# Kernel tuning notes

Measured on AMD Instinct MI355X. Metric: run time of the kernel, lower is better.

The kernel has to match this reference:

```python
import jax, jax.numpy as jnp
import numpy as np

EPS = 1e-8

def _conv(x, w, b=None):
    # NCHW conv, stride 1, SAME padding (k=3, pad=1)
    y = jax.lax.conv_general_dilated(x, w, (1, 1), 'SAME',
                                     dimension_numbers=('NCHW', 'OIHW', 'NCHW'))
    if b is not None:
        y = y + b[None, :, None, None]
    return y

def setup_inputs() -> dict:
    key = jax.random.key(0)
    ks = jax.random.split(key, 6)
    B, C, H, W = 512, 1024, 8, 8
    return {
        'x': jax.random.normal(ks[0], (B, C, H, W), jnp.float32),
        'w1_1': jax.random.normal(ks[1], (1, 1, 3, 3), jnp.float32) * 0.1,
        'w5': jax.random.normal(ks[2], (4, 2, 3, 3), jnp.float32) * 0.1,
        'b5': jax.random.normal(ks[3], (4,), jnp.float32) * 0.1,
        'w6': jax.random.normal(ks[4], (1, 4, 3, 3), jnp.float32) * 0.1,
        'b6': jax.random.normal(ks[5], (1,), jnp.float32) * 0.1,
    }

def reference(x, w1_1, w5, b5, w6, b6):
    B, C, H, W = x.shape  # H == W == 8 by module construction
    m = jnp.max(x, axis=1, keepdims=True)  # [B,1,H,W] channel max
    # 2x2 non-overlapping windows, torch unfold layout -> [B,1,(H/2)*(W/2),4]
    win = m.reshape(B, 1, H // 2, 2, W // 2, 2)
    win = win.transpose(0, 1, 2, 4, 3, 5).reshape(B, 1, (H // 2) * (W // 2), 4)
    # probabilistic pooling: clean inf/nan/negatives, sample per window
    winc = jnp.where(jnp.isinf(win) | jnp.isnan(win) | (win < 0), EPS, win)
    skey = jax.random.key(1)
    idx = jax.random.categorical(skey, winc, axis=-1)  # softmax(winc) multinomial
    mo2 = jnp.take_along_axis(winc, idx[..., None], axis=-1)[..., 0]
    mo2 = mo2.reshape(B, 1, H // 2, W // 2)
    # adaptive max/avg pool (4,4) on 8x8 == 2x2 pooling, reuse windows
    mo3 = win.max(axis=-1).reshape(B, 1, H // 2, W // 2)
    ao4 = win.mean(axis=-1).reshape(B, 1, H // 2, W // 2)
    out2 = 0.1 * mo2 + 0.6 * mo3 + 0.3 * ao4
    out2 = _conv(out2, w1_1)  # bias-free 1->1 conv
    out2 = jax.image.resize(out2, (B, 1, H, W), method='bilinear')  # align_corners=False
    out1 = jnp.concatenate([m, out2], axis=1)  # [B,2,H,W]
    gate = jax.nn.sigmoid(_conv(jax.nn.relu(_conv(out1, w5, b5)), w6, b6))  # [B,1,H,W]
    return jax.nn.relu(x * gate)
```

## Files before the change

kernel.cpp:

```cpp
#include <hip/hip_runtime.h>
#include <math.h>

#define C_DIM 1024
#define HW 64
#define F4_PER_BATCH 16384
#define EPSV 1e-8f
#define TINYF 1.17549435e-38f

typedef float vfloat4 __attribute__((ext_vector_type(4)));

__device__ __forceinline__ void threefry2x32_01(unsigned x0, unsigned x1,
                                                unsigned& o0, unsigned& o1) {
    const unsigned ks0 = 0u, ks1 = 1u, ks2 = 0x1BD11BDBu;
    x0 += ks0; x1 += ks1;
#define TF_R(r) { x0 += x1; x1 = (x1 << (r)) | (x1 >> (32 - (r))); x1 ^= x0; }
    TF_R(13) TF_R(15) TF_R(26) TF_R(6)
    x0 += ks1; x1 += ks2 + 1u;
    TF_R(17) TF_R(29) TF_R(16) TF_R(24)
    x0 += ks2; x1 += ks0 + 2u;
    TF_R(13) TF_R(15) TF_R(26) TF_R(6)
    x0 += ks0; x1 += ks1 + 3u;
    TF_R(17) TF_R(29) TF_R(16) TF_R(24)
    x0 += ks1; x1 += ks2 + 4u;
    TF_R(13) TF_R(15) TF_R(26) TF_R(6)
    x0 += ks2; x1 += ks0 + 5u;
#undef TF_R
    o0 = x0; o1 = x1;
}

__device__ __forceinline__ unsigned jax_random_bits(unsigned n) {
    unsigned o0, o1;
    threefry2x32_01(0u, n, o0, o1);
    return o0 ^ o1;
}

__device__ __forceinline__ bool bad_val(float v) {
    return ((__float_as_uint(v) & 0x7F800000u) == 0x7F800000u) || (v < 0.0f);
}

__device__ __forceinline__ unsigned enc_f32(float f) {
    unsigned b = __float_as_uint(f);
    return (b & 0x80000000u) ? ~b : (b | 0x80000000u);
}
__device__ __forceinline__ float dec_f32(unsigned u) {
    unsigned b = (u & 0x80000000u) ? (u ^ 0x80000000u) : ~u;
    return __uint_as_float(b);
}

__global__ __launch_bounds__(256) void sa_max_kernel(
    const float* __restrict__ x, unsigned* __restrict__ maxenc)
{
    const int bid = blockIdx.x;
    const int t = threadIdx.x;
    const int b = bid >> 2;
    const float4* __restrict__ xb = (const float4*)x + (size_t)bid * 4096;

    float4 pm = make_float4(-INFINITY, -INFINITY, -INFINITY, -INFINITY);
#pragma unroll 8
    for (int i = 0; i < 16; ++i) {
        float4 v = xb[t + 256 * i];
        pm.x = fmaxf(pm.x, v.x); pm.y = fmaxf(pm.y, v.y);
        pm.z = fmaxf(pm.z, v.z); pm.w = fmaxf(pm.w, v.w);
    }
#pragma unroll
    for (int off = 16; off <= 32; off <<= 1) {
        pm.x = fmaxf(pm.x, __shfl_xor(pm.x, off, 64));
        pm.y = fmaxf(pm.y, __shfl_xor(pm.y, off, 64));
        pm.z = fmaxf(pm.z, __shfl_xor(pm.z, off, 64));
        pm.w = fmaxf(pm.w, __shfl_xor(pm.w, off, 64));
    }
    __shared__ float4 red[4][16];
    const int wv = t >> 6, lane = t & 63;
    if (lane < 16) red[wv][lane] = pm;
    __syncthreads();
    if (t < 16) {
        float4 a = red[0][t];
#pragma unroll
        for (int w = 1; w < 4; ++w) {
            float4 o = red[w][t];
            a.x = fmaxf(a.x, o.x); a.y = fmaxf(a.y, o.y);
            a.z = fmaxf(a.z, o.z); a.w = fmaxf(a.w, o.w);
        }
        unsigned* dst = maxenc + b * 64 + t * 4;
        atomicMax(dst + 0, enc_f32(a.x));
        atomicMax(dst + 1, enc_f32(a.y));
        atomicMax(dst + 2, enc_f32(a.z));
        atomicMax(dst + 3, enc_f32(a.w));
    }
}

__global__ __launch_bounds__(64) void sa_middle_kernel(
    const unsigned* __restrict__ maxenc,
    const float* __restrict__ w11,
    const float* __restrict__ w5,
    const float* __restrict__ b5,
    const float* __restrict__ w6,
    const float* __restrict__ b6,
    float* __restrict__ gate_out)
{
    const int b = blockIdx.x;
    const int t = threadIdx.x;

    __shared__ float sm[64];
    __shared__ float sa16[16];
    __shared__ float sb16[16];
    __shared__ float so2[64];
    __shared__ float shid[4 * 64];

    sm[t] = dec_f32(maxenc[b * 64 + t]);
    __syncthreads();

    if (t < 16) {
        int h2 = t >> 2, w2 = t & 3;
        float win[4], winc[4], sg[4];
#pragma unroll
        for (int j = 0; j < 4; ++j) {
            int hh = 2 * h2 + (j >> 1), ww = 2 * w2 + (j & 1);
            float v = sm[hh * 8 + ww];
            win[j] = v;
            winc[j] = bad_val(v) ? EPSV : v;
            unsigned n = (unsigned)(b * 64 + t * 4 + j);
            unsigned bits = jax_random_bits(n);
            float f = __uint_as_float(0x3F800000u | (bits >> 9)) - 1.0f;
            float u = fmaxf(TINYF, f + TINYF);
            sg[j] = -logf(-logf(u));
        }
        int idx = 0;
        float best = winc[0] + sg[0];
#pragma unroll
        for (int j = 1; j < 4; ++j) {
            float s = winc[j] + sg[j];
            if (s > best) { best = s; idx = j; }
        }
        float mo2 = winc[idx];
        float mo3 = fmaxf(fmaxf(win[0], win[1]), fmaxf(win[2], win[3]));
        float ssum = ((win[0] + win[1]) + win[2]) + win[3];
        float ao4 = ssum * 0.25f;
        sa16[t] = 0.1f * mo2 + 0.6f * mo3 + 0.3f * ao4;
    }
    __syncthreads();

    if (t < 16) {
        int i = t >> 2, j = t & 3;
        float acc = 0.0f;
#pragma unroll
        for (int dy = -1; dy <= 1; ++dy) {
            int yy = i + dy;
            if (yy < 0 || yy > 3) continue;
#pragma unroll
            for (int dx = -1; dx <= 1; ++dx) {
                int xx = j + dx;
                if (xx < 0 || xx > 3) continue;
                acc += sa16[yy * 4 + xx] * w11[(dy + 1) * 3 + (dx + 1)];
            }
        }
        sb16[t] = acc;
    }
    __syncthreads();

    {
        int y = t >> 3, xx2 = t & 7;
        float sy = (y + 0.5f) * 0.5f - 0.5f;
        float sx = (xx2 + 0.5f) * 0.5f - 0.5f;
        float fy = fminf(fmaxf(sy, 0.0f), 3.0f);
        float fx = fminf(fmaxf(sx, 0.0f), 3.0f);
        int iy0 = (int)floorf(fy); int iy1 = min(iy0 + 1, 3); float ry = fy - (float)iy0;
        int ix0 = (int)floorf(fx); int ix1 = min(ix0 + 1, 3); float rx = fx - (float)ix0;
        float v00 = sb16[iy0 * 4 + ix0], v01 = sb16[iy0 * 4 + ix1];
        float v10 = sb16[iy1 * 4 + ix0], v11 = sb16[iy1 * 4 + ix1];
        float top = v00 * (1.0f - rx) + v01 * rx;
        float bot = v10 * (1.0f - rx) + v11 * rx;
        so2[t] = top * (1.0f - ry) + bot * ry;
    }
    __syncthreads();

    {
        int y = t >> 3, x2 = t & 7;
        float a0 = b5[0], a1 = b5[1], a2 = b5[2], a3 = b5[3];
#pragma unroll
        for (int dy = -1; dy <= 1; ++dy) {
            int yy = y + dy;
            if (yy < 0 || yy > 7) continue;
#pragma unroll
            for (int dx = -1; dx <= 1; ++dx) {
                int xx = x2 + dx;
                if (xx < 0 || xx > 7) continue;
                float i0 = sm[yy * 8 + xx];
                float i1 = so2[yy * 8 + xx];
                int kk = (dy + 1) * 3 + (dx + 1);
                a0 += i0 * w5[0 * 18 + kk] + i1 * w5[0 * 18 + 9 + kk];
                a1 += i0 * w5[1 * 18 + kk] + i1 * w5[1 * 18 + 9 + kk];
                a2 += i0 * w5[2 * 18 + kk] + i1 * w5[2 * 18 + 9 + kk];
                a3 += i0 * w5[3 * 18 + kk] + i1 * w5[3 * 18 + 9 + kk];
            }
        }
        shid[0 * 64 + t] = fmaxf(a0, 0.0f);
        shid[1 * 64 + t] = fmaxf(a1, 0.0f);
        shid[2 * 64 + t] = fmaxf(a2, 0.0f);
        shid[3 * 64 + t] = fmaxf(a3, 0.0f);
    }
    __syncthreads();

    {
        int y = t >> 3, x2 = t & 7;
        float acc = b6[0];
#pragma unroll
        for (int dy = -1; dy <= 1; ++dy) {
            int yy = y + dy;
            if (yy < 0 || yy > 7) continue;
#pragma unroll
            for (int dx = -1; dx <= 1; ++dx) {
                int xx = x2 + dx;
                if (xx < 0 || xx > 7) continue;
                int kk = (dy + 1) * 3 + (dx + 1);
                int p = yy * 8 + xx;
                acc += shid[0 * 64 + p] * w6[0 + kk]
                     + shid[1 * 64 + p] * w6[9 + kk]
                     + shid[2 * 64 + p] * w6[18 + kk]
                     + shid[3 * 64 + p] * w6[27 + kk];
            }
        }
        gate_out[b * 64 + t] = 1.0f / (1.0f + expf(-acc));
    }
}

__global__ __launch_bounds__(256) void sa_apply_kernel(
    const float* __restrict__ x,
    const float* __restrict__ gate,
    float* __restrict__ out)
{
    const int bid = blockIdx.x;
    const int t = threadIdx.x;
    const int b = bid >> 3;
    const size_t base = (size_t)bid * 2048;

    const vfloat4* __restrict__ x4 = (const vfloat4*)x;
    vfloat4* __restrict__ o4 = (vfloat4*)out;

    const float4 gv = ((const float4*)(gate + b * 64))[t & 15];

#pragma unroll
    for (int i = 0; i < 8; ++i) {
        size_t idx = base + t + 256 * i;
        vfloat4 v = x4[idx];
        vfloat4 o;
        o.x = fmaxf(v.x * gv.x, 0.0f);
        o.y = fmaxf(v.y * gv.y, 0.0f);
        o.z = fmaxf(v.z * gv.z, 0.0f);
        o.w = fmaxf(v.w * gv.w, 0.0f);
        __builtin_nontemporal_store(o, &o4[idx]);
    }
}

extern "C" void kernel_launch(void* const* d_in, const int* in_sizes, int n_in,
                              void* d_out, int out_size, void* d_ws, size_t ws_size,
                              hipStream_t stream) {
    const float* x   = (const float*)d_in[0];
    const float* w11 = (const float*)d_in[1];
    const float* w5  = (const float*)d_in[2];
    const float* b5  = (const float*)d_in[3];
    const float* w6  = (const float*)d_in[4];
    const float* b6  = (const float*)d_in[5];
    float* out = (float*)d_out;

    int B = in_sizes[0] / (C_DIM * HW);
    unsigned* maxenc = (unsigned*)d_ws;
    float* gate = (float*)d_ws + (size_t)B * 64;

    (void)hipMemsetAsync(maxenc, 0, (size_t)B * 64 * sizeof(unsigned), stream);
    sa_max_kernel<<<dim3(B * 4), dim3(256), 0, stream>>>(x, maxenc);
    sa_middle_kernel<<<dim3(B), dim3(64), 0, stream>>>(maxenc, w11, w5, b5, w6, b6, gate);
    sa_apply_kernel<<<dim3(B * 8), dim3(256), 0, stream>>>(x, gate, out);
}
```

Before: 266.4 us.

## Fuse gate computation into apply kernel and replace atomics with partial-max buffer

Drops the memset and the atomicMax reduction. The max kernel now writes per-block partial maxima to workspace, and the separate middle kernel is removed. Each apply block reduces the four partials for its batch, recomputes the small gate pipeline in its first wave, and keeps x loads in flight meanwhile. This cuts two launches and the atomic traffic, at the cost of redundant gate computation (8 blocks per batch) and more register pressure from holding 8 vectors. Stores also change from nontemporal to regular.

```diff
diff --git a/kernel.cpp b/kernel.cpp
--- a/kernel.cpp
+++ b/kernel.cpp
@@ -3,7 +3,6 @@
 
 #define C_DIM 1024
 #define HW 64
-#define F4_PER_BATCH 16384
 #define EPSV 1e-8f
 #define TINYF 1.17549435e-38f
 
@@ -38,25 +37,15 @@
     return ((__float_as_uint(v) & 0x7F800000u) == 0x7F800000u) || (v < 0.0f);
 }
 
-__device__ __forceinline__ unsigned enc_f32(float f) {
-    unsigned b = __float_as_uint(f);
-    return (b & 0x80000000u) ? ~b : (b | 0x80000000u);
-}
-__device__ __forceinline__ float dec_f32(unsigned u) {
-    unsigned b = (u & 0x80000000u) ? (u ^ 0x80000000u) : ~u;
-    return __uint_as_float(b);
-}
-
-__global__ __launch_bounds__(256) void sa_max_kernel(
-    const float* __restrict__ x, unsigned* __restrict__ maxenc)
+__global__ __launch_bounds__(256, 8) void sa_max_part(
+    const float* __restrict__ x, float4* __restrict__ part)
 {
     const int bid = blockIdx.x;
     const int t = threadIdx.x;
-    const int b = bid >> 2;
     const float4* __restrict__ xb = (const float4*)x + (size_t)bid * 4096;
 
     float4 pm = make_float4(-INFINITY, -INFINITY, -INFINITY, -INFINITY);
-#pragma unroll 8
+#pragma unroll
     for (int i = 0; i < 16; ++i) {
         float4 v = xb[t + 256 * i];
         pm.x = fmaxf(pm.x, v.x); pm.y = fmaxf(pm.y, v.y);
@@ -81,152 +70,18 @@
             a.x = fmaxf(a.x, o.x); a.y = fmaxf(a.y, o.y);
             a.z = fmaxf(a.z, o.z); a.w = fmaxf(a.w, o.w);
         }
-        unsigned* dst = maxenc + b * 64 + t * 4;
-        atomicMax(dst + 0, enc_f32(a.x));
-        atomicMax(dst + 1, enc_f32(a.y));
-        atomicMax(dst + 2, enc_f32(a.z));
-        atomicMax(dst + 3, enc_f32(a.w));
-    }
-}
-
-__global__ __launch_bounds__(64) void sa_middle_kernel(
-    const unsigned* __restrict__ maxenc,
+        part[bid * 16 + t] = a;
+    }
+}
+
+__global__ __launch_bounds__(256, 4) void sa_gate_apply(
+    const float* __restrict__ x,
+    const float* __restrict__ part,
     const float* __restrict__ w11,
     const float* __restrict__ w5,
     const float* __restrict__ b5,
     const float* __restrict__ w6,
     const float* __restrict__ b6,
-    float* __restrict__ gate_out)
-{
-    const int b = blockIdx.x;
-    const int t = threadIdx.x;
-
-    __shared__ float sm[64];
-    __shared__ float sa16[16];
-    __shared__ float sb16[16];
-    __shared__ float so2[64];
-    __shared__ float shid[4 * 64];
-
-    sm[t] = dec_f32(maxenc[b * 64 + t]);
-    __syncthreads();
-
-    if (t < 16) {
-        int h2 = t >> 2, w2 = t & 3;
-        float win[4], winc[4], sg[4];
-#pragma unroll
-        for (int j = 0; j < 4; ++j) {
-            int hh = 2 * h2 + (j >> 1), ww = 2 * w2 + (j & 1);
-            float v = sm[hh * 8 + ww];
-            win[j] = v;
-            winc[j] = bad_val(v) ? EPSV : v;
-            unsigned n = (unsigned)(b * 64 + t * 4 + j);
-            unsigned bits = jax_random_bits(n);
-            float f = __uint_as_float(0x3F800000u | (bits >> 9)) - 1.0f;
-            float u = fmaxf(TINYF, f + TINYF);
-            sg[j] = -logf(-logf(u));
-        }
-        int idx = 0;
-        float best = winc[0] + sg[0];
-#pragma unroll
-        for (int j = 1; j < 4; ++j) {
-            float s = winc[j] + sg[j];
-            if (s > best) { best = s; idx = j; }
-        }
-        float mo2 = winc[idx];
-        float mo3 = fmaxf(fmaxf(win[0], win[1]), fmaxf(win[2], win[3]));
-        float ssum = ((win[0] + win[1]) + win[2]) + win[3];
-        float ao4 = ssum * 0.25f;
-        sa16[t] = 0.1f * mo2 + 0.6f * mo3 + 0.3f * ao4;
-    }
-    __syncthreads();
-
-    if (t < 16) {
-        int i = t >> 2, j = t & 3;
-        float acc = 0.0f;
-#pragma unroll
-        for (int dy = -1; dy <= 1; ++dy) {
-            int yy = i + dy;
-            if (yy < 0 || yy > 3) continue;
-#pragma unroll
-            for (int dx = -1; dx <= 1; ++dx) {
-                int xx = j + dx;
-                if (xx < 0 || xx > 3) continue;
-                acc += sa16[yy * 4 + xx] * w11[(dy + 1) * 3 + (dx + 1)];
-            }
-        }
-        sb16[t] = acc;
-    }
-    __syncthreads();
-
-    {
-        int y = t >> 3, xx2 = t & 7;
-        float sy = (y + 0.5f) * 0.5f - 0.5f;
-        float sx = (xx2 + 0.5f) * 0.5f - 0.5f;
-        float fy = fminf(fmaxf(sy, 0.0f), 3.0f);
-        float fx = fminf(fmaxf(sx, 0.0f), 3.0f);
-        int iy0 = (int)floorf(fy); int iy1 = min(iy0 + 1, 3); float ry = fy - (float)iy0;
-        int ix0 = (int)floorf(fx); int ix1 = min(ix0 + 1, 3); float rx = fx - (float)ix0;
-        float v00 = sb16[iy0 * 4 + ix0], v01 = sb16[iy0 * 4 + ix1];
-        float v10 = sb16[iy1 * 4 + ix0], v11 = sb16[iy1 * 4 + ix1];
-        float top = v00 * (1.0f - rx) + v01 * rx;
-        float bot = v10 * (1.0f - rx) + v11 * rx;
-        so2[t] = top * (1.0f - ry) + bot * ry;
-    }
-    __syncthreads();
-
-    {
-        int y = t >> 3, x2 = t & 7;
-        float a0 = b5[0], a1 = b5[1], a2 = b5[2], a3 = b5[3];
-#pragma unroll
-        for (int dy = -1; dy <= 1; ++dy) {
-            int yy = y + dy;
-            if (yy < 0 || yy > 7) continue;
-#pragma unroll
-            for (int dx = -1; dx <= 1; ++dx) {
-                int xx = x2 + dx;
-                if (xx < 0 || xx > 7) continue;
-                float i0 = sm[yy * 8 + xx];
-                float i1 = so2[yy * 8 + xx];
-                int kk = (dy + 1) * 3 + (dx + 1);
-                a0 += i0 * w5[0 * 18 + kk] + i1 * w5[0 * 18 + 9 + kk];
-                a1 += i0 * w5[1 * 18 + kk] + i1 * w5[1 * 18 + 9 + kk];
-                a2 += i0 * w5[2 * 18 + kk] + i1 * w5[2 * 18 + 9 + kk];
-                a3 += i0 * w5[3 * 18 + kk] + i1 * w5[3 * 18 + 9 + kk];
-            }
-        }
-        shid[0 * 64 + t] = fmaxf(a0, 0.0f);
-        shid[1 * 64 + t] = fmaxf(a1, 0.0f);
-        shid[2 * 64 + t] = fmaxf(a2, 0.0f);
-        shid[3 * 64 + t] = fmaxf(a3, 0.0f);
-    }
-    __syncthreads();
-
-    {
-        int y = t >> 3, x2 = t & 7;
-        float acc = b6[0];
-#pragma unroll
-        for (int dy = -1; dy <= 1; ++dy) {
-            int yy = y + dy;
-            if (yy < 0 || yy > 7) continue;
-#pragma unroll
-            for (int dx = -1; dx <= 1; ++dx) {
-                int xx = x2 + dx;
-                if (xx < 0 || xx > 7) continue;
-                int kk = (dy + 1) * 3 + (dx + 1);
-                int p = yy * 8 + xx;
-                acc += shid[0 * 64 + p] * w6[0 + kk]
-                     + shid[1 * 64 + p] * w6[9 + kk]
-                     + shid[2 * 64 + p] * w6[18 + kk]
-                     + shid[3 * 64 + p] * w6[27 + kk];
-            }
-        }
-        gate_out[b * 64 + t] = 1.0f / (1.0f + expf(-acc));
-    }
-}
-
-__global__ __launch_bounds__(256) void sa_apply_kernel(
-    const float* __restrict__ x,
-    const float* __restrict__ gate,
     float* __restrict__ out)
 {
     const int bid = blockIdx.x;
@@ -237,18 +92,147 @@
     const vfloat4* __restrict__ x4 = (const vfloat4*)x;
     vfloat4* __restrict__ o4 = (vfloat4*)out;
 
-    const float4 gv = ((const float4*)(gate + b * 64))[t & 15];
-
+    vfloat4 v[8];
+#pragma unroll
+    for (int i = 0; i < 8; ++i) v[i] = x4[base + t + 256 * i];
+
+    __shared__ float sm[64];
+    __shared__ float sa16[16];
+    __shared__ float sb16[16];
+    __shared__ float so2[64];
+    __shared__ float shid[4 * 64];
+    __shared__ __align__(16) float sgate[64];
+
+    if (t < 64) {
+        const float* pb = part + b * 256;
+        sm[t] = fmaxf(fmaxf(pb[t], pb[64 + t]),
+                      fmaxf(pb[128 + t], pb[192 + t]));
+        __builtin_amdgcn_wave_barrier();
+
+        if (t < 16) {
+            int h2 = t >> 2, w2 = t & 3;
+            float win[4], winc[4], sg[4];
+#pragma unroll
+            for (int j = 0; j < 4; ++j) {
+                int hh = 2 * h2 + (j >> 1), ww = 2 * w2 + (j & 1);
+                float vv = sm[hh * 8 + ww];
+                win[j] = vv;
+                winc[j] = bad_val(vv) ? EPSV : vv;
+                unsigned n = (unsigned)(b * 64 + t * 4 + j);
+                unsigned bits = jax_random_bits(n);
+                float f = __uint_as_float(0x3F800000u | (bits >> 9)) - 1.0f;
+                float u = fmaxf(TINYF, f + TINYF);
+                sg[j] = -logf(-logf(u));
+            }
+            int idx = 0;
+            float best = winc[0] + sg[0];
+#pragma unroll
+            for (int j = 1; j < 4; ++j) {
+                float s = winc[j] + sg[j];
+                if (s > best) { best = s; idx = j; }
+            }
+            float mo2 = winc[idx];
+            float mo3 = fmaxf(fmaxf(win[0], win[1]), fmaxf(win[2], win[3]));
+            float ssum = ((win[0] + win[1]) + win[2]) + win[3];
+            float ao4 = ssum * 0.25f;
+            sa16[t] = 0.1f * mo2 + 0.6f * mo3 + 0.3f * ao4;
+        }
+        __builtin_amdgcn_wave_barrier();
+
+        if (t < 16) {
+            int i = t >> 2, j = t & 3;
+            float acc = 0.0f;
+#pragma unroll
+            for (int dy = -1; dy <= 1; ++dy) {
+                int yy = i + dy;
+                if (yy < 0 || yy > 3) continue;
+#pragma unroll
+                for (int dx = -1; dx <= 1; ++dx) {
+                    int xx = j + dx;
+                    if (xx < 0 || xx > 3) continue;
+                    acc += sa16[yy * 4 + xx] * w11[(dy + 1) * 3 + (dx + 1)];
+                }
+            }
+            sb16[t] = acc;
+        }
+        __builtin_amdgcn_wave_barrier();
+
+        {
+            int y = t >> 3, xx2 = t & 7;
+            float sy = (y + 0.5f) * 0.5f - 0.5f;
+            float sx = (xx2 + 0.5f) * 0.5f - 0.5f;
+            float fy = fminf(fmaxf(sy, 0.0f), 3.0f);
+            float fx = fminf(fmaxf(sx, 0.0f), 3.0f);
+            int iy0 = (int)floorf(fy); int iy1 = min(iy0 + 1, 3); float ry = fy - (float)iy0;
+            int ix0 = (int)floorf(fx); int ix1 = min(ix0 + 1, 3); float rx = fx - (float)ix0;
+            float v00 = sb16[iy0 * 4 + ix0], v01 = sb16[iy0 * 4 + ix1];
+            float v10 = sb16[iy1 * 4 + ix0], v11 = sb16[iy1 * 4 + ix1];
+            float top = v00 * (1.0f - rx) + v01 * rx;
+            float bot = v10 * (1.0f - rx) + v11 * rx;
+            so2[t] = top * (1.0f - ry) + bot * ry;
+        }
+        __builtin_amdgcn_wave_barrier();
+
+        {
+            int y = t >> 3, x2 = t & 7;
+            float a0 = b5[0], a1 = b5[1], a2 = b5[2], a3 = b5[3];
+#pragma unroll
+            for (int dy = -1; dy <= 1; ++dy) {
+                int yy = y + dy;
+                if (yy < 0 || yy > 7) continue;
+#pragma unroll
+                for (int dx = -1; dx <= 1; ++dx) {
+                    int xx = x2 + dx;
+                    if (xx < 0 || xx > 7) continue;
+                    float i0 = sm[yy * 8 + xx];
+                    float i1 = so2[yy * 8 + xx];
+                    int kk = (dy + 1) * 3 + (dx + 1);
+                    a0 += i0 * w5[0 * 18 + kk] + i1 * w5[0 * 18 + 9 + kk];
+                    a1 += i0 * w5[1 * 18 + kk] + i1 * w5[1 * 18 + 9 + kk];
+                    a2 += i0 * w5[2 * 18 + kk] + i1 * w5[2 * 18 + 9 + kk];
+                    a3 += i0 * w5[3 * 18 + kk] + i1 * w5[3 * 18 + 9 + kk];
+                }
+            }
+            shid[0 * 64 + t] = fmaxf(a0, 0.0f);
+            shid[1 * 64 + t] = fmaxf(a1, 0.0f);
+            shid[2 * 64 + t] = fmaxf(a2, 0.0f);
+            shid[3 * 64 + t] = fmaxf(a3, 0.0f);
+        }
+        __builtin_amdgcn_wave_barrier();
+
+        {
+            int y = t >> 3, x2 = t & 7;
+            float acc = b6[0];
+#pragma unroll
+            for (int dy = -1; dy <= 1; ++dy) {
+                int yy = y + dy;
+                if (yy < 0 || yy > 7) continue;
+#pragma unroll
+                for (int dx = -1; dx <= 1; ++dx) {
+                    int xx = x2 + dx;
+                    if (xx < 0 || xx > 7) continue;
+                    int kk = (dy + 1) * 3 + (dx + 1);
+                    int p = yy * 8 + xx;
+                    acc += shid[0 * 64 + p] * w6[0 + kk]
+                         + shid[1 * 64 + p] * w6[9 + kk]
+                         + shid[2 * 64 + p] * w6[18 + kk]
+                         + shid[3 * 64 + p] * w6[27 + kk];
+                }
+            }
+            sgate[t] = 1.0f / (1.0f + expf(-acc));
+        }
+    }
+    __syncthreads();
+
+    const float4 gv = ((const float4*)sgate)[t & 15];
 #pragma unroll
     for (int i = 0; i < 8; ++i) {
-        size_t idx = base + t + 256 * i;
-        vfloat4 v = x4[idx];
         vfloat4 o;
-        o.x = fmaxf(v.x * gv.x, 0.0f);
-        o.y = fmaxf(v.y * gv.y, 0.0f);
-        o.z = fmaxf(v.z * gv.z, 0.0f);
-        o.w = fmaxf(v.w * gv.w, 0.0f);
-        __builtin_nontemporal_store(o, &o4[idx]);
+        o.x = fmaxf(v[i].x * gv.x, 0.0f);
+        o.y = fmaxf(v[i].y * gv.y, 0.0f);
+        o.z = fmaxf(v[i].z * gv.z, 0.0f);
+        o.w = fmaxf(v[i].w * gv.w, 0.0f);
+        o4[base + t + 256 * i] = o;
     }
 }
 
@@ -264,11 +248,9 @@
     float* out = (float*)d_out;
 
     int B = in_sizes[0] / (C_DIM * HW);
-    unsigned* maxenc = (unsigned*)d_ws;
-    float* gate = (float*)d_ws + (size_t)B * 64;
-
-    (void)hipMemsetAsync(maxenc, 0, (size_t)B * 64 * sizeof(unsigned), stream);
-    sa_max_kernel<<<dim3(B * 4), dim3(256), 0, stream>>>(x, maxenc);
-    sa_middle_kernel<<<dim3(B), dim3(64), 0, stream>>>(maxenc, w11, w5, b5, w6, b6, gate);
-    sa_apply_kernel<<<dim3(B * 8), dim3(256), 0, stream>>>(x, gate, out);
-}
+    float4* part = (float4*)d_ws;
+
+    sa_max_part<<<dim3(B * 4), dim3(256), 0, stream>>>(x, part);
+    sa_gate_apply<<<dim3(B * 8), dim3(256), 0, stream>>>(
+        x, (const float*)part, w11, w5, b5, w6, b6, out);
+}
```

After: 260.7 us. -2.2%, faster.
